# Kernel tuning notes

Hardware: AMD Instinct MI355X
Metric: run time of the kernel (lower is better)

## Reference

```python
import jax, jax.numpy as jnp
import numpy as np

N, D, K = 131072, 64, 512
COMMITMENT_COST = 0.25
DECAY = 0.99
EPSILON = 1e-05


def setup_inputs() -> dict:
    key = jax.random.key(0)
    k1, k2, k3 = jax.random.split(key, 3)
    return {
        "inputs": jax.random.normal(k1, (N, D), dtype=jnp.float32),
        "embedding_weight": jax.random.normal(k2, (K, D), dtype=jnp.float32),
        "ema_w": jax.random.normal(k3, (K, D), dtype=jnp.float32),
        "ema_cluster_size": jnp.zeros((K,), dtype=jnp.float32),
    }


def reference(inputs, embedding_weight, ema_w, ema_cluster_size):
    num_embeddings = embedding_weight.shape[0]
    distances = (
        jnp.sum(inputs ** 2, axis=1, keepdims=True)
        + jnp.sum(embedding_weight ** 2, axis=1)
        - 2.0 * jnp.matmul(inputs, embedding_weight.T)
    )
    encoding_indices = jnp.argmin(distances, axis=1)  # [N]
    # dense one-hot (returned by the module); float32 instead of torch double
    encodings = jax.nn.one_hot(encoding_indices, num_embeddings, dtype=jnp.float32)
    # encodings @ W is just a codebook gather
    quantized = jnp.take(embedding_weight, encoding_indices, axis=0)  # [N, D]

    # ---- EMA codebook update (training path; all detached from autodiff) ----
    counts = jax.ops.segment_sum(
        jnp.ones((inputs.shape[0],), dtype=jnp.float32),
        encoding_indices, num_segments=num_embeddings)  # == encodings.sum(0)
    new_cluster_size = ema_cluster_size * DECAY + (1.0 - DECAY) * counts
    n = jnp.sum(new_cluster_size)
    new_cluster_size = (new_cluster_size + EPSILON) / (n + num_embeddings * EPSILON) * n
    # dw = encodings^T @ inputs -> scatter-add of inputs per code
    dw = jax.ops.segment_sum(inputs, encoding_indices, num_segments=num_embeddings)
    new_ema_w = ema_w * DECAY + (1.0 - DECAY) * dw
    new_embedding = new_ema_w / new_cluster_size[:, None]
    new_cluster_size = jax.lax.stop_gradient(new_cluster_size)
    new_ema_w = jax.lax.stop_gradient(new_ema_w)
    new_embedding = jax.lax.stop_gradient(new_embedding)

    # commitment loss (quantized detached)
    e_latent_loss = jnp.mean((jax.lax.stop_gradient(quantized) - inputs) ** 2)
    loss = COMMITMENT_COST * e_latent_loss
    # straight-through estimator
    quantized_st = inputs + jax.lax.stop_gradient(quantized - inputs)

    avg_probs = jnp.mean(encodings, axis=0)
    perplexity = jnp.exp(-jnp.sum(avg_probs * jnp.log(avg_probs + 1e-10)))
    return (loss, quantized_st, perplexity, encodings,
            new_embedding, new_cluster_size, new_ema_w)
```

## Files before the change

kernel.cpp:

```cpp
#include <hip/hip_runtime.h>

#define NROWS 131072
#define DDIM  64
#define KCODE 512

#define QUANT_OFF 1LL
#define PERP_OFF  8388609LL
#define ENC_OFF   8388610LL
#define EMB_OFF   75497474LL
#define CS_OFF    75530242LL
#define EMAW_OFF  75530754LL

#define WS_COUNTS 0
#define WS_NEGWN  512
#define WS_SSE    1024
#define WS_DW     1040
#define WS_ZERO_FLOATS 33808
#define WS_OFF    33808
#define WS_POS    34320
#define WS_IDX    34832
#define WS_BUCKET 165904
#define WS_WHI    296976
#define WS_WMID   313360
#define WS_WLO    329744

using short8 = __attribute__((ext_vector_type(8))) short;
using f32x4  = __attribute__((ext_vector_type(4))) float;
using f32x2  = __attribute__((ext_vector_type(2))) float;

#define MFMA(a, b, c) __builtin_amdgcn_mfma_f32_16x16x32_bf16((a), (b), (c), 0, 0, 0)

__device__ inline unsigned short bf16_rne(float x) {
    unsigned u = __float_as_uint(x);
    unsigned r = u + 0x7FFFu + ((u >> 16) & 1u);
    return (unsigned short)(r >> 16);
}
__device__ inline float bf16_to_f(unsigned short h) {
    return __uint_as_float((unsigned)h << 16);
}
__device__ inline void split3(const float* v, short8& h8, short8& m8, short8& l8) {
#pragma unroll
    for (int j = 0; j < 8; ++j) {
        float x = v[j];
        unsigned short h = bf16_rne(x);
        float m_ = x - bf16_to_f(h);
        unsigned short m = bf16_rne(m_);
        float l_ = m_ - bf16_to_f(m);
        unsigned short l = bf16_rne(l_);
        h8[j] = (short)h; m8[j] = (short)m; l8[j] = (short)l;
    }
}

__global__ __launch_bounds__(256) void prep_kernel(
    const float* __restrict__ W, ushort* __restrict__ whi,
    ushort* __restrict__ wmid, ushort* __restrict__ wlo,
    float* __restrict__ negwn) {
    if (blockIdx.x == 8) {
        for (int k = threadIdx.x; k < KCODE; k += 256) {
            const float4* wr = reinterpret_cast<const float4*>(&W[(size_t)k * DDIM]);
            float s = 0.f;
#pragma unroll
            for (int i = 0; i < DDIM / 4; ++i) {
                float4 v = wr[i];
                s += v.x * v.x + v.y * v.y + v.z * v.z + v.w * v.w;
            }
            negwn[k] = -0.5f * s;
        }
        return;
    }
    int t = blockIdx.x * 256 + threadIdx.x;
    int lane = t & 63;
    int code = (t >> 6) * 16 + (lane & 15);
    int kbase = (lane >> 4) * 8;
    int obase = t * 16;
#pragma unroll
    for (int kh = 0; kh < 2; ++kh) {
        float xbuf[8];
#pragma unroll
        for (int j = 0; j < 8; ++j) xbuf[j] = W[code * 64 + kh * 32 + kbase + j];
        short8 h8, m8, l8;
        split3(xbuf, h8, m8, l8);
#pragma unroll
        for (int j = 0; j < 8; ++j) {
            whi[obase + kh * 8 + j]  = (ushort)h8[j];
            wmid[obase + kh * 8 + j] = (ushort)m8[j];
            wlo[obase + kh * 8 + j]  = (ushort)l8[j];
        }
    }
}

__global__ __launch_bounds__(256) void vq_main_kernel(
    const float* __restrict__ X, const ushort* __restrict__ WHI,
    const ushort* __restrict__ WMID, const ushort* __restrict__ WLO,
    const float* __restrict__ negwn, const float* __restrict__ W,
    float* __restrict__ counts, float* __restrict__ sse_g,
    int* __restrict__ idx_out, float* __restrict__ outq,
    float* __restrict__ enc) {

    __shared__ int rowIdx[128];
    const int tid = threadIdx.x;
    const int wave = tid >> 6, lane = tid & 63;
    const int col = lane & 15, kg = lane >> 4;
    const int row0 = blockIdx.x * 128;
    const int rowbase = row0 + wave * 32;

    float* encblk = enc + ((size_t)row0 << 9);
    const f32x4 z4 = {0.f, 0.f, 0.f, 0.f};
    const f32x2 z2 = {0.f, 0.f};

    short8 xh[2][2], xm[2][2], xl[2][2];
#pragma unroll
    for (int t = 0; t < 2; ++t) {
        int row = rowbase + t * 16 + col;
#pragma unroll
        for (int kh = 0; kh < 2; ++kh) {
            const float4* p = reinterpret_cast<const float4*>(&X[row * 64 + kh * 32 + kg * 8]);
            float4 a = p[0], b = p[1];
            float xbuf[8] = {a.x, a.y, a.z, a.w, b.x, b.y, b.z, b.w};
            split3(xbuf, xh[t][kh], xm[t][kh], xl[t][kh]);
        }
    }

    float bestV[2][4]; int bestC[2][4];
#pragma unroll
    for (int t = 0; t < 2; ++t)
#pragma unroll
        for (int i = 0; i < 4; ++i) { bestV[t][i] = -3.4e38f; bestC[t][i] = 0; }

    for (int c = 0; c < 32; ++c) {
        {
            int v0 = c * 512 + tid;
            __builtin_nontemporal_store(z4, reinterpret_cast<f32x4*>(encblk + 2 + 4 * v0));
            int v1 = v0 + 256;
            if (v1 < 16383)
                __builtin_nontemporal_store(z4, reinterpret_cast<f32x4*>(encblk + 2 + 4 * v1));
            if (c == 0) {
                if (tid == 0)
                    __builtin_nontemporal_store(z2, reinterpret_cast<f32x2*>(encblk));
                if (tid == 1)
                    __builtin_nontemporal_store(z2, reinterpret_cast<f32x2*>(encblk + 65534));
            }
        }

        const short8* ph = reinterpret_cast<const short8*>(&WHI[(c * 64 + lane) * 16]);
        const short8* pm = reinterpret_cast<const short8*>(&WMID[(c * 64 + lane) * 16]);
        const short8* pl = reinterpret_cast<const short8*>(&WLO[(c * 64 + lane) * 16]);
        short8 wh0 = ph[0], wh1 = ph[1];
        short8 wm0 = pm[0], wm1 = pm[1];
        short8 wl0 = pl[0], wl1 = pl[1];
        float wn = negwn[c * 16 + col];
#pragma unroll
        for (int t = 0; t < 2; ++t) {
            f32x4 acc = {0.f, 0.f, 0.f, 0.f};
            acc = MFMA(xh[t][0], wl0, acc); acc = MFMA(xh[t][1], wl1, acc);
            acc = MFMA(xl[t][0], wh0, acc); acc = MFMA(xl[t][1], wh1, acc);
            acc = MFMA(xm[t][0], wm0, acc); acc = MFMA(xm[t][1], wm1, acc);
            acc = MFMA(xh[t][0], wm0, acc); acc = MFMA(xh[t][1], wm1, acc);
            acc = MFMA(xm[t][0], wh0, acc); acc = MFMA(xm[t][1], wh1, acc);
            acc = MFMA(xh[t][0], wh0, acc); acc = MFMA(xh[t][1], wh1, acc);
#pragma unroll
            for (int i = 0; i < 4; ++i) {
                float r = acc[i] + wn;
                if (r > bestV[t][i]) { bestV[t][i] = r; bestC[t][i] = c; }
            }
        }
    }

#pragma unroll
    for (int t = 0; t < 2; ++t)
#pragma unroll
        for (int i = 0; i < 4; ++i) {
            float v = bestV[t][i];
            int ix = bestC[t][i] * 16 + col;
#pragma unroll
            for (int m = 1; m <= 8; m <<= 1) {
                float ov = __shfl_xor(v, m);
                int   oi = __shfl_xor(ix, m);
                if (ov > v || (ov == v && oi < ix)) { v = ov; ix = oi; }
            }
            if (col == 0) rowIdx[wave * 32 + t * 16 + kg * 4 + i] = ix;
        }
    __syncthreads();

    float ssel = 0.f;
    for (int u = tid; u < 128 * 16; u += 256) {
        int r = u >> 4, d4 = (u & 15) << 2;
        int ix = rowIdx[r];
        float4 wv = *reinterpret_cast<const float4*>(&W[ix * 64 + d4]);
        float4 xv = *reinterpret_cast<const float4*>(&X[(size_t)(row0 + r) * 64 + d4]);
        float dx = wv.x - xv.x, dy = wv.y - xv.y, dz = wv.z - xv.z, dw4 = wv.w - xv.w;
        ssel += dx * dx + dy * dy + dz * dz + dw4 * dw4;
        size_t ob = (size_t)(row0 + r) * 64 + d4;
        outq[ob + 0] = xv.x + dx;
        outq[ob + 1] = xv.y + dy;
        outq[ob + 2] = xv.z + dz;
        outq[ob + 3] = xv.w + dw4;
    }
#pragma unroll
    for (int m = 32; m >= 1; m >>= 1) ssel += __shfl_xor(ssel, m);
    if (lane == 0) atomicAdd(sse_g, ssel);

    if (tid < 128) {
        int ix = rowIdx[tid];
        idx_out[row0 + tid] = ix;
        atomicAdd(&counts[ix], 1.0f);
        enc[((size_t)(row0 + tid) << 9) + ix] = 1.0f;
    }
}

__global__ void prefix_kernel(const float* __restrict__ counts,
                              int* __restrict__ off, int* __restrict__ pos) {
    __shared__ int tmp[512];
    int t = threadIdx.x;
    int c = (int)counts[t];
    tmp[t] = c;
    __syncthreads();
    int val = c;
    for (int s = 1; s < 512; s <<= 1) {
        int add = (t >= s) ? tmp[t - s] : 0;
        __syncthreads();
        val += add; tmp[t] = val;
        __syncthreads();
    }
    int excl = val - c;
    off[t] = excl; pos[t] = excl;
}

__global__ void scatter_kernel(const int* __restrict__ idx, int* __restrict__ pos,
                               int* __restrict__ bucket) {
    int i = blockIdx.x * 256 + threadIdx.x;
    int k = idx[i];
    int p = atomicAdd(&pos[k], 1);
    bucket[p] = (k << 17) | i;
}

__global__ __launch_bounds__(256) void dwsum_kernel(
    const float* __restrict__ X, const int* __restrict__ bucket,
    float* __restrict__ dw) {
    const int lane = threadIdx.x & 63;
    const int gwave = (blockIdx.x * 256 + threadIdx.x) >> 6;
    const int r0 = gwave * 16;
    int v = bucket[r0];
    int k = v >> 17, row = v & 0x1FFFF;
    float acc = 0.f;
#pragma unroll
    for (int i = 0; i < 16; ++i) {
        acc += X[(size_t)row * 64 + lane];
        if (i + 1 < 16) {
            int nv = bucket[r0 + i + 1];
            int nk = nv >> 17, nrow = nv & 0x1FFFF;
            if (nk != k) {
                atomicAdd(&dw[k * 64 + lane], acc);
                acc = 0.f; k = nk;
            }
            row = nrow;
        }
    }
    atomicAdd(&dw[k * 64 + lane], acc);
}

__global__ __launch_bounds__(512) void finalize_kernel(
    const float* __restrict__ ema_w, const float* __restrict__ ema_cs,
    const float* __restrict__ counts, const float* __restrict__ dw,
    const float* __restrict__ sse_g, float* __restrict__ out) {

    __shared__ float red[512];
    __shared__ float cs_sh[512];
    int t = threadIdx.x;

    float cnt = counts[t];
    float raw = ema_cs[t] * 0.99f + 0.01f * cnt;
    red[t] = raw;
    __syncthreads();
    for (int s = 256; s > 0; s >>= 1) {
        if (t < s) red[t] += red[t + s];
        __syncthreads();
    }
    float n = red[0];
    __syncthreads();

    float ncs = (raw + 1e-5f) / (n + (float)KCODE * 1e-5f) * n;
    out[CS_OFF + t] = ncs;
    cs_sh[t] = ncs;

    float avg = cnt / (float)NROWS;
    red[t] = avg * logf(avg + 1e-10f);
    __syncthreads();
    for (int s = 256; s > 0; s >>= 1) {
        if (t < s) red[t] += red[t + s];
        __syncthreads();
    }
    if (t == 0) {
        out[PERP_OFF] = expf(-red[0]);
        out[0] = 0.25f * sse_g[0] / ((float)NROWS * (float)DDIM);
    }
    __syncthreads();

    for (int i = t; i < KCODE * DDIM; i += 512) {
        float ne = ema_w[i] * 0.99f + 0.01f * dw[i];
        out[EMAW_OFF + i] = ne;
        out[EMB_OFF + i] = ne / cs_sh[i >> 6];
    }
}

extern "C" void kernel_launch(void* const* d_in, const int* in_sizes, int n_in,
                              void* d_out, int out_size, void* d_ws, size_t ws_size,
                              hipStream_t stream) {
    const float* X      = (const float*)d_in[0];
    const float* W      = (const float*)d_in[1];
    const float* ema_w  = (const float*)d_in[2];
    const float* ema_cs = (const float*)d_in[3];
    float* out = (float*)d_out;
    float* ws  = (float*)d_ws;

    float*  counts = ws + WS_COUNTS;
    float*  negwn  = ws + WS_NEGWN;
    float*  sse    = ws + WS_SSE;
    float*  dw     = ws + WS_DW;
    int*    off    = (int*)(ws + WS_OFF);
    int*    pos    = (int*)(ws + WS_POS);
    int*    idx    = (int*)(ws + WS_IDX);
    int*    bucket = (int*)(ws + WS_BUCKET);
    ushort* whi    = (ushort*)(ws + WS_WHI);
    ushort* wmid   = (ushort*)(ws + WS_WMID);
    ushort* wlo    = (ushort*)(ws + WS_WLO);

    (void)hipMemsetAsync(d_ws, 0, (size_t)WS_ZERO_FLOATS * sizeof(float), stream);

    prep_kernel<<<9, 256, 0, stream>>>(W, whi, wmid, wlo, negwn);
    vq_main_kernel<<<NROWS / 128, 256, 0, stream>>>(X, whi, wmid, wlo, negwn, W,
                                                    counts, sse, idx,
                                                    out + QUANT_OFF, out + ENC_OFF);
    prefix_kernel<<<1, 512, 0, stream>>>(counts, off, pos);
    scatter_kernel<<<NROWS / 256, 256, 0, stream>>>(idx, pos, bucket);
    dwsum_kernel<<<NROWS / 16 / 4, 256, 0, stream>>>(X, bucket, dw);
    finalize_kernel<<<1, 512, 0, stream>>>(ema_w, ema_cs, counts, dw, sse, out);
}
```

Baseline: 265.6 us.

## Fuse dw segment-sum into main kernel via direct float atomics

Replaces the prefix/scatter/bucketed dwsum pipeline with per-element float atomicAdd into the dw accumulator inside the main VQ kernel, reusing the X values already loaded for the quantized output. This removes three kernel launches, the index and bucket buffers, and the extra pass that re-reads X. In exchange it issues N*D global float atomics, which can contend heavily on popular codes, and the summation order becomes nondeterministic.

```diff
diff --git a/kernel.cpp b/kernel.cpp
--- a/kernel.cpp
+++ b/kernel.cpp
@@ -16,10 +16,6 @@
 #define WS_SSE    1024
 #define WS_DW     1040
 #define WS_ZERO_FLOATS 33808
-#define WS_OFF    33808
-#define WS_POS    34320
-#define WS_IDX    34832
-#define WS_BUCKET 165904
 #define WS_WHI    296976
 #define WS_WMID   313360
 #define WS_WLO    329744
@@ -94,7 +90,7 @@
     const ushort* __restrict__ WMID, const ushort* __restrict__ WLO,
     const float* __restrict__ negwn, const float* __restrict__ W,
     float* __restrict__ counts, float* __restrict__ sse_g,
-    int* __restrict__ idx_out, float* __restrict__ outq,
+    float* __restrict__ dwg, float* __restrict__ outq,
     float* __restrict__ enc) {
 
     __shared__ int rowIdx[128];
@@ -195,6 +191,11 @@
         outq[ob + 1] = xv.y + dy;
         outq[ob + 2] = xv.z + dz;
         outq[ob + 3] = xv.w + dw4;
+        size_t db = (size_t)ix * 64 + d4;
+        atomicAdd(&dwg[db + 0], xv.x);
+        atomicAdd(&dwg[db + 1], xv.y);
+        atomicAdd(&dwg[db + 2], xv.z);
+        atomicAdd(&dwg[db + 3], xv.w);
     }
 #pragma unroll
     for (int m = 32; m >= 1; m >>= 1) ssel += __shfl_xor(ssel, m);
@@ -202,61 +203,9 @@
 
     if (tid < 128) {
         int ix = rowIdx[tid];
-        idx_out[row0 + tid] = ix;
         atomicAdd(&counts[ix], 1.0f);
         enc[((size_t)(row0 + tid) << 9) + ix] = 1.0f;
     }
-}
-
-__global__ void prefix_kernel(const float* __restrict__ counts,
-                              int* __restrict__ off, int* __restrict__ pos) {
-    __shared__ int tmp[512];
-    int t = threadIdx.x;
-    int c = (int)counts[t];
-    tmp[t] = c;
-    __syncthreads();
-    int val = c;
-    for (int s = 1; s < 512; s <<= 1) {
-        int add = (t >= s) ? tmp[t - s] : 0;
-        __syncthreads();
-        val += add; tmp[t] = val;
-        __syncthreads();
-    }
-    int excl = val - c;
-    off[t] = excl; pos[t] = excl;
-}
-
-__global__ void scatter_kernel(const int* __restrict__ idx, int* __restrict__ pos,
-                               int* __restrict__ bucket) {
-    int i = blockIdx.x * 256 + threadIdx.x;
-    int k = idx[i];
-    int p = atomicAdd(&pos[k], 1);
-    bucket[p] = (k << 17) | i;
-}
-
-__global__ __launch_bounds__(256) void dwsum_kernel(
-    const float* __restrict__ X, const int* __restrict__ bucket,
-    float* __restrict__ dw) {
-    const int lane = threadIdx.x & 63;
-    const int gwave = (blockIdx.x * 256 + threadIdx.x) >> 6;
-    const int r0 = gwave * 16;
-    int v = bucket[r0];
-    int k = v >> 17, row = v & 0x1FFFF;
-    float acc = 0.f;
-#pragma unroll
-    for (int i = 0; i < 16; ++i) {
-        acc += X[(size_t)row * 64 + lane];
-        if (i + 1 < 16) {
-            int nv = bucket[r0 + i + 1];
-            int nk = nv >> 17, nrow = nv & 0x1FFFF;
-            if (nk != k) {
-                atomicAdd(&dw[k * 64 + lane], acc);
-                acc = 0.f; k = nk;
-            }
-            row = nrow;
-        }
-    }
-    atomicAdd(&dw[k * 64 + lane], acc);
 }
 
 __global__ __launch_bounds__(512) void finalize_kernel(
@@ -317,10 +266,6 @@
     float*  negwn  = ws + WS_NEGWN;
     float*  sse    = ws + WS_SSE;
     float*  dw     = ws + WS_DW;
-    int*    off    = (int*)(ws + WS_OFF);
-    int*    pos    = (int*)(ws + WS_POS);
-    int*    idx    = (int*)(ws + WS_IDX);
-    int*    bucket = (int*)(ws + WS_BUCKET);
     ushort* whi    = (ushort*)(ws + WS_WHI);
     ushort* wmid   = (ushort*)(ws + WS_WMID);
     ushort* wlo    = (ushort*)(ws + WS_WLO);
@@ -329,10 +274,7 @@
 
     prep_kernel<<<9, 256, 0, stream>>>(W, whi, wmid, wlo, negwn);
     vq_main_kernel<<<NROWS / 128, 256, 0, stream>>>(X, whi, wmid, wlo, negwn, W,
-                                                    counts, sse, idx,
+                                                    counts, sse, dw,
                                                     out + QUANT_OFF, out + ENC_OFF);
-    prefix_kernel<<<1, 512, 0, stream>>>(counts, off, pos);
-    scatter_kernel<<<NROWS / 256, 256, 0, stream>>>(idx, pos, bucket);
-    dwsum_kernel<<<NROWS / 16 / 4, 256, 0, stream>>>(X, bucket, dw);
     finalize_kernel<<<1, 512, 0, stream>>>(ema_w, ema_cs, counts, dw, sse, out);
 }
```

Result: slower. 462.0 us (+73.9%).
